# Optimization experiments

Hardware: AMD Instinct MI355X
Metric: run time of the kernel (lower is better)

## Reference

```python
import jax, jax.numpy as jnp
import numpy as np

N_NODES = 200000
N_EDGES = 600000
EMB = 128
HID = 128
N_RELS = 64
N_MOTIFS = 512
N_CENTERS = 256
N_NODE_CLASSES = 16


def _linear_params(key, out_dim, in_dim):
    kw, kb = jax.random.split(key)
    s = 1.0 / np.sqrt(in_dim)
    w = jax.random.uniform(kw, (out_dim, in_dim), jnp.float32, -s, s)
    b = jax.random.uniform(kb, (out_dim,), jnp.float32, -s, s)
    return w, b


def setup_inputs() -> dict:
    key = jax.random.key(0)
    ks = jax.random.split(key, 12)
    lin_w, lin_b = _linear_params(ks[2], HID, EMB)
    conv1_w, conv1_b = _linear_params(ks[3], HID, HID)
    conv2_w, conv2_b = _linear_params(ks[4], HID, HID)
    edge_w, edge_b = _linear_params(ks[5], N_RELS, 2 * HID)
    motif_w, motif_b = _linear_params(ks[6], N_MOTIFS, HID)
    node_w, node_b = _linear_params(ks[7], N_NODE_CLASSES, HID)
    return {
        "node_emb": jax.random.normal(ks[0], (N_NODES, EMB), jnp.float32),
        "rel_emb": jax.random.normal(ks[1], (N_RELS, EMB), jnp.float32),
        "lin_w": lin_w, "lin_b": lin_b,
        "conv1_w": conv1_w, "conv1_b": conv1_b,
        "conv2_w": conv2_w, "conv2_b": conv2_b,
        "edge_w": edge_w, "edge_b": edge_b,
        "motif_w": motif_w, "motif_b": motif_b,
        "node_w": node_w, "node_b": node_b,
        "node_ids": jnp.arange(N_NODES, dtype=jnp.int32),
        "rel_ids": jax.random.randint(ks[8], (N_EDGES,), 0, N_RELS, jnp.int32),
        "center_mol_idx": jax.random.randint(ks[9], (N_CENTERS,), 0, N_NODES, jnp.int32),
        "edge_index": jax.random.randint(ks[10], (2, N_EDGES), 0, N_NODES, jnp.int32),
    }


def _gine_conv(x, edge_index, edge_attr, w, b):
    # PyG GINEConv (eps=0): nn((1+eps)*x + sum_j relu(x_j + e_ji))
    src, dst = edge_index[0], edge_index[1]
    msg = jax.nn.relu(x[src] + edge_attr)               # [E, H]
    agg = jax.ops.segment_sum(msg, dst, num_segments=x.shape[0])  # [N, H]
    return (agg + x) @ w.T + b


def reference(node_emb, rel_emb, lin_w, lin_b, conv1_w, conv1_b,
              conv2_w, conv2_b, edge_w, edge_b, motif_w, motif_b,
              node_w, node_b, node_ids, rel_ids, center_mol_idx, edge_index):
    x = node_emb[node_ids]            # [N, EMB]
    edge_attr = rel_emb[rel_ids]      # [E, EMB]
    x = x @ lin_w.T + lin_b           # [N, H]
    edge_attr = edge_attr @ lin_w.T + lin_b  # [E, H]
    x = _gine_conv(x, edge_index, edge_attr, conv1_w, conv1_b)
    x = jax.nn.relu(x)
    x = _gine_conv(x, edge_index, edge_attr, conv2_w, conv2_b)
    edge_pred_input = jnp.concatenate([x[edge_index[0]], x[edge_index[1]]], axis=1)  # [E, 2H]
    edge_class = edge_pred_input @ edge_w.T + edge_b       # [E, num_rels]
    center = x[center_mol_idx]                             # [C, H]
    motif_pred = center @ motif_w.T + motif_b              # [C, num_motifs]
    node_class = x @ node_w.T + node_b                     # [N, 16]
    return (edge_class, motif_pred, node_class)
```

## Files before the change

kernel.cpp:

```cpp
#include <hip/hip_runtime.h>
#include <hip/hip_bf16.h>

#define N_NODES 200000
#define N_EDGES 600000
#define EMB 128
#define HID 128
#define N_RELS 64
#define N_MOTIFS 512
#define N_CENTERS 256
#define NCLS 16

#define SCAN_C 512
#define NB_SCAN ((N_NODES + SCAN_C - 1) / SCAN_C)

typedef unsigned short u16;
typedef __attribute__((ext_vector_type(8))) short short8;
typedef __attribute__((ext_vector_type(4))) float f32x4;

__device__ __forceinline__ float bf2f(u16 u) {
    unsigned int i = ((unsigned int)u) << 16;
    float f; __builtin_memcpy(&f, &i, 4); return f;
}
__device__ __forceinline__ u16 f2bf(float f) {
    unsigned int x; __builtin_memcpy(&x, &f, 4);
    x += 0x7fffu + ((x >> 16) & 1u);
    return (u16)(x >> 16);
}

#define O_LINW   0
#define O_LINB   16384
#define O_C1W    16512
#define O_C1B    32896
#define O_C2W    33024
#define O_C2B    49408
#define O_EW     49536
#define O_EB     65920
#define O_MW     65984
#define O_MB     131520
#define O_NW     132032
#define O_NB     134080
#define N_WB     134096

__global__ void k_pre(const float* __restrict__ rel_emb,
                      const float* __restrict__ lw, const float* __restrict__ lb,
                      const float* __restrict__ c1w, const float* __restrict__ c1b,
                      const float* __restrict__ c2w, const float* __restrict__ c2b,
                      const float* __restrict__ ew, const float* __restrict__ eb,
                      const float* __restrict__ mw, const float* __restrict__ mb,
                      const float* __restrict__ nw, const float* __restrict__ nb,
                      float* __restrict__ rel_lin, u16* __restrict__ wb)
{
    if (blockIdx.x < 64) {
        __shared__ float e[EMB];
        const int r = blockIdx.x, h = threadIdx.x;
        e[h] = rel_emb[r * EMB + h];
        __syncthreads();
        const float* wr = lw + (size_t)h * EMB;
        float acc = lb[h];
        #pragma unroll
        for (int k0 = 0; k0 < EMB; k0 += 4) {
            f32x4 wv = *(const f32x4*)(wr + k0);
            #pragma unroll
            for (int j = 0; j < 4; ++j) acc += e[k0 + j] * wv[j];
        }
        rel_lin[r * HID + h] = acc;
        return;
    }
    const int t = (blockIdx.x - 64) * 128 + threadIdx.x;
    if (t >= N_WB) return;
    float v;
    if      (t < O_LINB) v = lw[t - O_LINW];
    else if (t < O_C1W)  v = lb[t - O_LINB];
    else if (t < O_C1B)  v = c1w[t - O_C1W];
    else if (t < O_C2W)  v = c1b[t - O_C1B];
    else if (t < O_C2B)  v = c2w[t - O_C2W];
    else if (t < O_EW)   v = c2b[t - O_C2B];
    else if (t < O_EB)   v = ew[t - O_EW];
    else if (t < O_MW)   v = eb[t - O_EB];
    else if (t < O_MB)   v = mw[t - O_MW];
    else if (t < O_NW)   v = mb[t - O_MB];
    else if (t < O_NB)   v = nw[t - O_NW];
    else                 v = nb[t - O_NB];
    wb[t] = f2bf(v);
}

__global__ void k_hist(const int* __restrict__ dst, int* __restrict__ deg)
{
    const int e = blockIdx.x * 256 + threadIdx.x;
    if (e < N_EDGES) atomicAdd(&deg[dst[e]], 1);
}

__global__ void k_scan1(const int* __restrict__ deg, int* __restrict__ bsum)
{
    __shared__ int sd[256];
    const int t = threadIdx.x, base = blockIdx.x * SCAN_C;
    int v = 0;
    int i0 = base + t, i1 = base + 256 + t;
    if (i0 < N_NODES) v += deg[i0];
    if (i1 < N_NODES) v += deg[i1];
    sd[t] = v; __syncthreads();
    for (int s = 128; s > 0; s >>= 1) {
        if (t < s) sd[t] += sd[t + s];
        __syncthreads();
    }
    if (t == 0) bsum[blockIdx.x] = sd[0];
}

__global__ void k_scan2(int* __restrict__ bsum, int* __restrict__ row_ptr)
{
    __shared__ int sh[512];
    const int t = threadIdx.x;
    int v = (t < NB_SCAN) ? bsum[t] : 0;
    sh[t] = v;
    for (int off = 1; off < 512; off <<= 1) {
        __syncthreads();
        int a = (t >= off) ? sh[t - off] : 0;
        __syncthreads();
        sh[t] += a;
    }
    __syncthreads();
    if (t < NB_SCAN) bsum[t] = sh[t] - v;
    if (t == 511) row_ptr[N_NODES] = sh[511];
}

__global__ void k_scan3(const int* __restrict__ deg, const int* __restrict__ bsum,
                        int* __restrict__ row_ptr)
{
    __shared__ int sh[256];
    const int t = threadIdx.x, base = blockIdx.x * SCAN_C;
    const int i0 = base + 2 * t, i1 = i0 + 1;
    int d0 = (i0 < N_NODES) ? deg[i0] : 0;
    int d1 = (i1 < N_NODES) ? deg[i1] : 0;
    int p = d0 + d1;
    sh[t] = p;
    for (int off = 1; off < 256; off <<= 1) {
        __syncthreads();
        int a = (t >= off) ? sh[t - off] : 0;
        __syncthreads();
        sh[t] += a;
    }
    __syncthreads();
    const int off = bsum[blockIdx.x] + sh[t] - p;
    if (i0 < N_NODES) row_ptr[i0] = off;
    if (i1 < N_NODES) row_ptr[i1] = off + d0;
}

__global__ void k_fill(const int* __restrict__ src, const int* __restrict__ dst,
                       const int* __restrict__ rid, const int* __restrict__ row_ptr,
                       int* __restrict__ cur, int* __restrict__ srcrid)
{
    const int e = blockIdx.x * 256 + threadIdx.x;
    if (e >= N_EDGES) return;
    const int d = dst[e];
    const int pos = row_ptr[d] + atomicAdd(&cur[d], 1);
    srcrid[pos] = src[e] * 64 + rid[e];
}

__global__ __launch_bounds__(256) void k_lin(
    const float* __restrict__ emb, const int* __restrict__ ids,
    const u16* __restrict__ w, const u16* __restrict__ bias,
    u16* __restrict__ out)
{
    const int wid = threadIdx.x >> 6, lane = threadIdx.x & 63;
    const int r15 = lane & 15, kg = (lane >> 4) * 8;
    const int arow = blockIdx.x * 64 + wid * 16 + r15;
    const int srow = ids[arow];
    const float* ar = emb + (size_t)srow * EMB + kg;
    short8 a[4];
    #pragma unroll
    for (int kk = 0; kk < 4; ++kk) {
        f32x4 a0 = *(const f32x4*)(ar + kk * 32);
        f32x4 a1 = *(const f32x4*)(ar + kk * 32 + 4);
        short8 t;
        #pragma unroll
        for (int j = 0; j < 4; ++j) { t[j] = (short)f2bf(a0[j]); t[4 + j] = (short)f2bf(a1[j]); }
        a[kk] = t;
    }
    f32x4 acc[8];
    #pragma unroll
    for (int nb = 0; nb < 8; ++nb) acc[nb] = (f32x4){0.f, 0.f, 0.f, 0.f};
    #pragma unroll
    for (int nb = 0; nb < 8; ++nb) {
        const u16* wr = w + (size_t)(nb * 16 + r15) * EMB + kg;
        #pragma unroll
        for (int kk = 0; kk < 4; ++kk) {
            short8 bv = *(const short8*)(wr + kk * 32);
            acc[nb] = __builtin_amdgcn_mfma_f32_16x16x32_bf16(a[kk], bv, acc[nb], 0, 0, 0);
        }
    }
    const int ob = blockIdx.x * 64 + wid * 16 + (lane >> 4) * 4;
    #pragma unroll
    for (int nb = 0; nb < 8; ++nb) {
        const int col = nb * 16 + r15;
        const float bn = bf2f(bias[col]);
        #pragma unroll
        for (int r = 0; r < 4; ++r)
            out[(size_t)(ob + r) * HID + col] = f2bf(acc[nb][r] + bn);
    }
}

__global__ __launch_bounds__(256) void k_fuse(
    const u16* __restrict__ x, const float* __restrict__ rel_lin,
    const int* __restrict__ row_ptr, const int* __restrict__ srcrid,
    const u16* __restrict__ w, const u16* __restrict__ bias,
    u16* __restrict__ out, const int do_relu)
{
    __shared__ u16 rel[N_RELS * 128];
    {
        const int r = threadIdx.x >> 2;
        #pragma unroll
        for (int k = 0; k < 4; ++k) {
            const int ch = (threadIdx.x & 3) * 4 + k;
            const float* sp = rel_lin + r * HID + ch * 8;
            short8 t;
            #pragma unroll
            for (int j = 0; j < 8; ++j) t[j] = (short)f2bf(sp[j]);
            *(short8*)(&rel[r * 128 + ((ch ^ (r & 7)) * 8)]) = t;
        }
    }
    __syncthreads();

    const int wid = threadIdx.x >> 6, lane = threadIdx.x & 63;
    const int r15 = lane & 15;
    const int kq  = lane >> 4;
    const int kg  = kq * 8;
    const int n = blockIdx.x * 64 + wid * 16 + r15;
    const int pbeg = row_ptr[n], pend = row_ptr[n + 1];

    float acc[32];
    #pragma unroll
    for (int j = 0; j < 32; ++j) acc[j] = 0.f;

    int p = pbeg;
    for (; p + 2 <= pend; p += 2) {
        const int v0 = srcrid[p], v1 = srcrid[p + 1];
        const int s0 = v0 >> 6, r0 = v0 & 63;
        const int s1 = v1 >> 6, r1 = v1 & 63;
        const u16* xp0 = x + (size_t)s0 * HID + kg;
        const u16* xp1 = x + (size_t)s1 * HID + kg;
        short8 xv0[4], xv1[4], rv0[4], rv1[4];
        #pragma unroll
        for (int kk = 0; kk < 4; ++kk) {
            xv0[kk] = *(const short8*)(xp0 + kk * 32);
            xv1[kk] = *(const short8*)(xp1 + kk * 32);
            rv0[kk] = *(const short8*)(&rel[r0 * 128 + (((kq + kk * 4) ^ (r0 & 7)) * 8)]);
            rv1[kk] = *(const short8*)(&rel[r1 * 128 + (((kq + kk * 4) ^ (r1 & 7)) * 8)]);
        }
        #pragma unroll
        for (int kk = 0; kk < 4; ++kk)
            #pragma unroll
            for (int j = 0; j < 8; ++j) {
                acc[kk * 8 + j] += fmaxf(bf2f((u16)xv0[kk][j]) + bf2f((u16)rv0[kk][j]), 0.f);
                acc[kk * 8 + j] += fmaxf(bf2f((u16)xv1[kk][j]) + bf2f((u16)rv1[kk][j]), 0.f);
            }
    }
    if (p < pend) {
        const int v = srcrid[p];
        const int s = v >> 6, r = v & 63;
        const u16* xp = x + (size_t)s * HID + kg;
        #pragma unroll
        for (int kk = 0; kk < 4; ++kk) {
            short8 xv = *(const short8*)(xp + kk * 32);
            short8 rv = *(const short8*)(&rel[r * 128 + (((kq + kk * 4) ^ (r & 7)) * 8)]);
            #pragma unroll
            for (int j = 0; j < 8; ++j)
                acc[kk * 8 + j] += fmaxf(bf2f((u16)xv[j]) + bf2f((u16)rv[j]), 0.f);
        }
    }

    short8 a[4];
    {
        const u16* xp = x + (size_t)n * HID + kg;
        #pragma unroll
        for (int kk = 0; kk < 4; ++kk) {
            short8 xv = *(const short8*)(xp + kk * 32);
            short8 t;
            #pragma unroll
            for (int j = 0; j < 8; ++j) t[j] = (short)f2bf(acc[kk * 8 + j] + bf2f((u16)xv[j]));
            a[kk] = t;
        }
    }

    f32x4 accm[8];
    #pragma unroll
    for (int nb = 0; nb < 8; ++nb) accm[nb] = (f32x4){0.f, 0.f, 0.f, 0.f};
    #pragma unroll
    for (int nb = 0; nb < 8; ++nb) {
        const u16* wr = w + (size_t)(nb * 16 + r15) * HID + kg;
        #pragma unroll
        for (int kk = 0; kk < 4; ++kk) {
            short8 bv = *(const short8*)(wr + kk * 32);
            accm[nb] = __builtin_amdgcn_mfma_f32_16x16x32_bf16(a[kk], bv, accm[nb], 0, 0, 0);
        }
    }
    const int ob = blockIdx.x * 64 + wid * 16 + (lane >> 4) * 4;
    #pragma unroll
    for (int nb = 0; nb < 8; ++nb) {
        const int col = nb * 16 + r15;
        const float bn = bf2f(bias[col]);
        #pragma unroll
        for (int r = 0; r < 4; ++r) {
            float v = accm[nb][r] + bn;
            if (do_relu) v = fmaxf(v, 0.f);
            out[(size_t)(ob + r) * HID + col] = f2bf(v);
        }
    }
}

__global__ __launch_bounds__(256) void k_heads(
    const u16* __restrict__ x2, const u16* __restrict__ ew,
    const u16* __restrict__ nw, const u16* __restrict__ nbias,
    u16* __restrict__ y, float* __restrict__ node_out)
{
    const int wid = threadIdx.x >> 6, lane = threadIdx.x & 63;
    const int r15 = lane & 15, kg = (lane >> 4) * 8;
    const int arow = blockIdx.x * 64 + wid * 16 + r15;
    const u16* xr = x2 + (size_t)arow * HID + kg;
    short8 a[4];
    #pragma unroll
    for (int kk = 0; kk < 4; ++kk) a[kk] = *(const short8*)(xr + kk * 32);

    f32x4 accs[4], accd[4], accn;
    #pragma unroll
    for (int nb = 0; nb < 4; ++nb) {
        accs[nb] = (f32x4){0.f, 0.f, 0.f, 0.f};
        accd[nb] = (f32x4){0.f, 0.f, 0.f, 0.f};
    }
    accn = (f32x4){0.f, 0.f, 0.f, 0.f};

    #pragma unroll
    for (int nb = 0; nb < 4; ++nb) {
        const u16* wr = ew + (size_t)(nb * 16 + r15) * 256 + kg;
        #pragma unroll
        for (int kk = 0; kk < 4; ++kk) {
            short8 bs = *(const short8*)(wr + kk * 32);
            short8 bd = *(const short8*)(wr + 128 + kk * 32);
            accs[nb] = __builtin_amdgcn_mfma_f32_16x16x32_bf16(a[kk], bs, accs[nb], 0, 0, 0);
            accd[nb] = __builtin_amdgcn_mfma_f32_16x16x32_bf16(a[kk], bd, accd[nb], 0, 0, 0);
        }
    }
    {
        const u16* wr = nw + (size_t)r15 * HID + kg;
        #pragma unroll
        for (int kk = 0; kk < 4; ++kk) {
            short8 bv = *(const short8*)(wr + kk * 32);
            accn = __builtin_amdgcn_mfma_f32_16x16x32_bf16(a[kk], bv, accn, 0, 0, 0);
        }
    }

    const int ob = blockIdx.x * 64 + wid * 16 + (lane >> 4) * 4;
    #pragma unroll
    for (int nb = 0; nb < 4; ++nb) {
        const int col = nb * 16 + r15;
        #pragma unroll
        for (int r = 0; r < 4; ++r) {
            y[(size_t)(ob + r) * 128 + col] = f2bf(accs[nb][r]);
            y[(size_t)(ob + r) * 128 + 64 + col] = f2bf(accd[nb][r]);
        }
    }
    const float bn = bf2f(nbias[r15]);
    #pragma unroll
    for (int r = 0; r < 4; ++r)
        node_out[(size_t)(ob + r) * NCLS + r15] = accn[r] + bn;
}

__global__ __launch_bounds__(256) void k_eout(
    const u16* __restrict__ y, const int* __restrict__ src, const int* __restrict__ dst,
    const float* __restrict__ eb, float* __restrict__ out)
{
    const int t = blockIdx.x * 256 + threadIdx.x;
    const int e = t >> 2;
    const int qq = (t & 3) * 16;
    const int s = src[e], d = dst[e];
    const u16* ys = y + (size_t)s * 128 + qq;
    const u16* yd = y + (size_t)d * 128 + 64 + qq;
    const float* ebp = eb + qq;
    float* op = out + (size_t)e * 64 + qq;
    #pragma unroll
    for (int c = 0; c < 2; ++c) {
        short8 vs = *(const short8*)(ys + c * 8);
        short8 vd = *(const short8*)(yd + c * 8);
        #pragma unroll
        for (int h = 0; h < 2; ++h) {
            f32x4 vb = *(const f32x4*)(ebp + c * 8 + h * 4);
            f32x4 r;
            #pragma unroll
            for (int j = 0; j < 4; ++j)
                r[j] = bf2f((u16)vs[h * 4 + j]) + bf2f((u16)vd[h * 4 + j]) + vb[j];
            *(f32x4*)(op + c * 8 + h * 4) = r;
        }
    }
}

__global__ void k_motif(const u16* __restrict__ x2, const int* __restrict__ centers,
                        const u16* __restrict__ mw, const u16* __restrict__ mb,
                        float* __restrict__ out)
{
    __shared__ float xs[HID];
    const int c = blockIdx.x, m = threadIdx.x;
    if (m < HID) xs[m] = bf2f(x2[(size_t)centers[c] * HID + m]);
    __syncthreads();
    const u16* wr = mw + (size_t)m * HID;
    float acc = bf2f(mb[m]);
    #pragma unroll
    for (int k0 = 0; k0 < HID; k0 += 8) {
        short8 wv = *(const short8*)(wr + k0);
        #pragma unroll
        for (int j = 0; j < 8; ++j) acc += xs[k0 + j] * bf2f((u16)wv[j]);
    }
    out[(size_t)c * N_MOTIFS + m] = acc;
}

extern "C" void kernel_launch(void* const* d_in, const int* in_sizes, int n_in,
                              void* d_out, int out_size, void* d_ws, size_t ws_size,
                              hipStream_t stream)
{
    const float* node_emb = (const float*)d_in[0];
    const float* rel_emb  = (const float*)d_in[1];
    const float* lin_w    = (const float*)d_in[2];
    const float* lin_b    = (const float*)d_in[3];
    const float* conv1_w  = (const float*)d_in[4];
    const float* conv1_b  = (const float*)d_in[5];
    const float* conv2_w  = (const float*)d_in[6];
    const float* conv2_b  = (const float*)d_in[7];
    const float* edge_w   = (const float*)d_in[8];
    const float* edge_b   = (const float*)d_in[9];
    const float* motif_w  = (const float*)d_in[10];
    const float* motif_b  = (const float*)d_in[11];
    const float* node_w   = (const float*)d_in[12];
    const float* node_b   = (const float*)d_in[13];
    const int* node_ids = (const int*)d_in[14];
    const int* rel_ids  = (const int*)d_in[15];
    const int* centers  = (const int*)d_in[16];
    const int* src      = (const int*)d_in[17];
    const int* dst      = ((const int*)d_in[17]) + N_EDGES;

    char* ws = (char*)d_ws;
    float* rel_lin = (float*)ws;
    u16*   wb      = (u16*)(ws + 32768);
    u16*   x0      = (u16*)(ws + 524288);
    u16*   x1      = (u16*)(ws + 524288 + 51200000);
    u16*   y       = (u16*)(ws + 524288 + 2 * 51200000);
    char*  csr     = ws + 524288 + 2 * 51200000 + 102400000;
    int*   deg     = (int*)csr;
    int*   cur     = (int*)(csr + 800000);
    int*   row_ptr = (int*)(csr + 1600000);
    int*   srcrid  = (int*)(csr + 2400032);
    int*   bsum    = (int*)(csr + 4800032);
    u16*   x2      = x0;

    float* out_edge  = (float*)d_out;
    float* out_motif = out_edge + (size_t)N_EDGES * 64;
    float* out_node  = out_motif + (size_t)N_CENTERS * N_MOTIFS;

    k_pre<<<64 + (N_WB + 127) / 128, 128, 0, stream>>>(
        rel_emb, lin_w, lin_b, conv1_w, conv1_b, conv2_w, conv2_b,
        edge_w, edge_b, motif_w, motif_b, node_w, node_b, rel_lin, wb);
    hipMemsetAsync(deg, 0, 1600000, stream);

    k_hist<<<(N_EDGES + 255) / 256, 256, 0, stream>>>(dst, deg);
    k_scan1<<<NB_SCAN, 256, 0, stream>>>(deg, bsum);
    k_scan2<<<1, 512, 0, stream>>>(bsum, row_ptr);
    k_scan3<<<NB_SCAN, 256, 0, stream>>>(deg, bsum, row_ptr);
    k_fill<<<(N_EDGES + 255) / 256, 256, 0, stream>>>(src, dst, rel_ids, row_ptr, cur, srcrid);

    k_lin<<<N_NODES / 64, 256, 0, stream>>>(node_emb, node_ids, wb + O_LINW, wb + O_LINB, x0);
    k_fuse<<<N_NODES / 64, 256, 0, stream>>>(x0, rel_lin, row_ptr, srcrid,
                                             wb + O_C1W, wb + O_C1B, x1, 1);
    k_fuse<<<N_NODES / 64, 256, 0, stream>>>(x1, rel_lin, row_ptr, srcrid,
                                             wb + O_C2W, wb + O_C2B, x2, 0);
    k_heads<<<N_NODES / 64, 256, 0, stream>>>(x2, wb + O_EW, wb + O_NW, wb + O_NB, y, out_node);
    k_eout<<<(N_EDGES * 4) / 256, 256, 0, stream>>>(y, src, dst, edge_b, out_edge);
    k_motif<<<N_CENTERS, N_MOTIFS, 0, stream>>>(x2, centers, wb + O_MW, wb + O_MB, out_motif);
}
```

Measured before the change: 469.6 us.

## Split GINE message computation into a separate edge-parallel kernel before aggregation

The gather of x[src] plus the relation embedding and the ReLU move out of the per-node aggregation kernel into a new edge-parallel kernel, k_msg2. It writes bf16 messages in CSR order into the output buffer, used as scratch. The aggregation kernel then streams those messages contiguously with no LDS relation table and no random gathers. This is meant to turn the irregular per-node gather into a well-parallelised edge pass. The cost is an extra write and read of about 150MB of messages per layer, plus two more kernel launches.

```diff
diff --git a/kernel.cpp b/kernel.cpp
--- a/kernel.cpp
+++ b/kernel.cpp
@@ -48,7 +48,8 @@
                       const float* __restrict__ ew, const float* __restrict__ eb,
                       const float* __restrict__ mw, const float* __restrict__ mb,
                       const float* __restrict__ nw, const float* __restrict__ nb,
-                      float* __restrict__ rel_lin, u16* __restrict__ wb)
+                      float* __restrict__ rel_lin, u16* __restrict__ rel_bf,
+                      u16* __restrict__ wb)
 {
     if (blockIdx.x < 64) {
         __shared__ float e[EMB];
@@ -64,6 +65,7 @@
             for (int j = 0; j < 4; ++j) acc += e[k0 + j] * wv[j];
         }
         rel_lin[r * HID + h] = acc;
+        rel_bf[r * HID + h] = f2bf(acc);
         return;
     }
     const int t = (blockIdx.x - 64) * 128 + threadIdx.x;
@@ -199,31 +201,39 @@
     }
 }
 
-__global__ __launch_bounds__(256) void k_fuse(
-    const u16* __restrict__ x, const float* __restrict__ rel_lin,
-    const int* __restrict__ row_ptr, const int* __restrict__ srcrid,
+__global__ __launch_bounds__(256) void k_msg2(
+    const u16* __restrict__ x, const u16* __restrict__ relb,
+    const int* __restrict__ srcrid, u16* __restrict__ msg)
+{
+    const int t = blockIdx.x * 256 + threadIdx.x;
+    const int p = t >> 2;
+    const int q = (t & 3) * 32;
+    const int v = srcrid[p];
+    const int s = v >> 6, r = v & 63;
+    const u16* xp = x + (size_t)s * HID + q;
+    const u16* rp = relb + r * HID + q;
+    u16* mp = msg + (size_t)p * HID + q;
+    #pragma unroll
+    for (int c = 0; c < 4; ++c) {
+        short8 xv = *(const short8*)(xp + c * 8);
+        short8 rv = *(const short8*)(rp + c * 8);
+        short8 o;
+        #pragma unroll
+        for (int j = 0; j < 8; ++j)
+            o[j] = (short)f2bf(fmaxf(bf2f((u16)xv[j]) + bf2f((u16)rv[j]), 0.f));
+        *(short8*)(mp + c * 8) = o;
+    }
+}
+
+__global__ __launch_bounds__(256) void k_fuse2(
+    const u16* __restrict__ x, const u16* __restrict__ msg,
+    const int* __restrict__ row_ptr,
     const u16* __restrict__ w, const u16* __restrict__ bias,
     u16* __restrict__ out, const int do_relu)
 {
-    __shared__ u16 rel[N_RELS * 128];
-    {
-        const int r = threadIdx.x >> 2;
-        #pragma unroll
-        for (int k = 0; k < 4; ++k) {
-            const int ch = (threadIdx.x & 3) * 4 + k;
-            const float* sp = rel_lin + r * HID + ch * 8;
-            short8 t;
-            #pragma unroll
-            for (int j = 0; j < 8; ++j) t[j] = (short)f2bf(sp[j]);
-            *(short8*)(&rel[r * 128 + ((ch ^ (r & 7)) * 8)]) = t;
-        }
-    }
-    __syncthreads();
-
     const int wid = threadIdx.x >> 6, lane = threadIdx.x & 63;
     const int r15 = lane & 15;
-    const int kq  = lane >> 4;
-    const int kg  = kq * 8;
+    const int kg = (lane >> 4) * 8;
     const int n = blockIdx.x * 64 + wid * 16 + r15;
     const int pbeg = row_ptr[n], pend = row_ptr[n + 1];
 
@@ -233,38 +243,25 @@
 
     int p = pbeg;
     for (; p + 2 <= pend; p += 2) {
-        const int v0 = srcrid[p], v1 = srcrid[p + 1];
-        const int s0 = v0 >> 6, r0 = v0 & 63;
-        const int s1 = v1 >> 6, r1 = v1 & 63;
-        const u16* xp0 = x + (size_t)s0 * HID + kg;
-        const u16* xp1 = x + (size_t)s1 * HID + kg;
-        short8 xv0[4], xv1[4], rv0[4], rv1[4];
-        #pragma unroll
-        for (int kk = 0; kk < 4; ++kk) {
-            xv0[kk] = *(const short8*)(xp0 + kk * 32);
-            xv1[kk] = *(const short8*)(xp1 + kk * 32);
-            rv0[kk] = *(const short8*)(&rel[r0 * 128 + (((kq + kk * 4) ^ (r0 & 7)) * 8)]);
-            rv1[kk] = *(const short8*)(&rel[r1 * 128 + (((kq + kk * 4) ^ (r1 & 7)) * 8)]);
-        }
+        const u16* m0 = msg + (size_t)p * HID + kg;
+        const u16* m1 = m0 + HID;
+        short8 v0[4], v1[4];
+        #pragma unroll
+        for (int kk = 0; kk < 4; ++kk) { v0[kk] = *(const short8*)(m0 + kk * 32);
+                                         v1[kk] = *(const short8*)(m1 + kk * 32); }
         #pragma unroll
         for (int kk = 0; kk < 4; ++kk)
             #pragma unroll
-            for (int j = 0; j < 8; ++j) {
-                acc[kk * 8 + j] += fmaxf(bf2f((u16)xv0[kk][j]) + bf2f((u16)rv0[kk][j]), 0.f);
-                acc[kk * 8 + j] += fmaxf(bf2f((u16)xv1[kk][j]) + bf2f((u16)rv1[kk][j]), 0.f);
-            }
+            for (int j = 0; j < 8; ++j)
+                acc[kk * 8 + j] += bf2f((u16)v0[kk][j]) + bf2f((u16)v1[kk][j]);
     }
     if (p < pend) {
-        const int v = srcrid[p];
-        const int s = v >> 6, r = v & 63;
-        const u16* xp = x + (size_t)s * HID + kg;
-        #pragma unroll
-        for (int kk = 0; kk < 4; ++kk) {
-            short8 xv = *(const short8*)(xp + kk * 32);
-            short8 rv = *(const short8*)(&rel[r * 128 + (((kq + kk * 4) ^ (r & 7)) * 8)]);
+        const u16* m0 = msg + (size_t)p * HID + kg;
+        #pragma unroll
+        for (int kk = 0; kk < 4; ++kk) {
+            short8 v0 = *(const short8*)(m0 + kk * 32);
             #pragma unroll
-            for (int j = 0; j < 8; ++j)
-                acc[kk * 8 + j] += fmaxf(bf2f((u16)xv[j]) + bf2f((u16)rv[j]), 0.f);
+            for (int j = 0; j < 8; ++j) acc[kk * 8 + j] += bf2f((u16)v0[j]);
         }
     }
 
@@ -438,10 +435,11 @@
     char* ws = (char*)d_ws;
     float* rel_lin = (float*)ws;
     u16*   wb      = (u16*)(ws + 32768);
+    u16*   rel_bf  = (u16*)(ws + 393216);
     u16*   x0      = (u16*)(ws + 524288);
     u16*   x1      = (u16*)(ws + 524288 + 51200000);
     u16*   y       = (u16*)(ws + 524288 + 2 * 51200000);
-    char*  csr     = ws + 524288 + 2 * 51200000 + 102400000;
+    char*  csr     = ws + 524288 + 3 * 51200000;
     int*   deg     = (int*)csr;
     int*   cur     = (int*)(csr + 800000);
     int*   row_ptr = (int*)(csr + 1600000);
@@ -453,9 +451,11 @@
     float* out_motif = out_edge + (size_t)N_EDGES * 64;
     float* out_node  = out_motif + (size_t)N_CENTERS * N_MOTIFS;
 
+    u16* msg = (u16*)d_out;
+
     k_pre<<<64 + (N_WB + 127) / 128, 128, 0, stream>>>(
         rel_emb, lin_w, lin_b, conv1_w, conv1_b, conv2_w, conv2_b,
-        edge_w, edge_b, motif_w, motif_b, node_w, node_b, rel_lin, wb);
+        edge_w, edge_b, motif_w, motif_b, node_w, node_b, rel_lin, rel_bf, wb);
     hipMemsetAsync(deg, 0, 1600000, stream);
 
     k_hist<<<(N_EDGES + 255) / 256, 256, 0, stream>>>(dst, deg);
@@ -465,10 +465,14 @@
     k_fill<<<(N_EDGES + 255) / 256, 256, 0, stream>>>(src, dst, rel_ids, row_ptr, cur, srcrid);
 
     k_lin<<<N_NODES / 64, 256, 0, stream>>>(node_emb, node_ids, wb + O_LINW, wb + O_LINB, x0);
-    k_fuse<<<N_NODES / 64, 256, 0, stream>>>(x0, rel_lin, row_ptr, srcrid,
-                                             wb + O_C1W, wb + O_C1B, x1, 1);
-    k_fuse<<<N_NODES / 64, 256, 0, stream>>>(x1, rel_lin, row_ptr, srcrid,
-                                             wb + O_C2W, wb + O_C2B, x2, 0);
+
+    k_msg2<<<(N_EDGES * 4) / 256, 256, 0, stream>>>(x0, rel_bf, srcrid, msg);
+    k_fuse2<<<N_NODES / 64, 256, 0, stream>>>(x0, msg, row_ptr,
+                                              wb + O_C1W, wb + O_C1B, x1, 1);
+    k_msg2<<<(N_EDGES * 4) / 256, 256, 0, stream>>>(x1, rel_bf, srcrid, msg);
+    k_fuse2<<<N_NODES / 64, 256, 0, stream>>>(x1, msg, row_ptr,
+                                              wb + O_C2W, wb + O_C2B, x2, 0);
+
     k_heads<<<N_NODES / 64, 256, 0, stream>>>(x2, wb + O_EW, wb + O_NW, wb + O_NB, y, out_node);
     k_eout<<<(N_EDGES * 4) / 256, 256, 0, stream>>>(y, src, dst, edge_b, out_edge);
     k_motif<<<N_CENTERS, N_MOTIFS, 0, stream>>>(x2, centers, wb + O_MW, wb + O_MB, out_motif);
```

After: 558.4 us. +18.9%, slower.
